# Kernel optimization log

Hardware: AMD Instinct MI355X
Metric: run time of the kernel (lower is better)

The kernel has to match this reference:

```python
import jax, jax.numpy as jnp
import numpy as np

N_NODES = 100000
N_EDGES = 1600000
MOTIF_DIM = 32
HIDDEN = 64


def setup_inputs() -> dict:
    key = jax.random.key(0)
    k1, k2, k3, k4 = jax.random.split(key, 4)
    motif_x = jax.random.normal(k1, (N_NODES, MOTIF_DIM), dtype=jnp.float32)
    edge_index = jax.random.randint(k2, (2, N_EDGES), 0, N_NODES, dtype=jnp.int64)
    in_dim = 4 * MOTIF_DIM
    W1 = jax.random.normal(k3, (in_dim, HIDDEN), dtype=jnp.float32) / np.sqrt(in_dim)
    b1 = jnp.zeros((HIDDEN,), dtype=jnp.float32)
    W2 = jax.random.normal(k4, (HIDDEN, 1), dtype=jnp.float32) / np.sqrt(HIDDEN)
    b2 = jnp.zeros((1,), dtype=jnp.float32)
    return {"motif_x": motif_x, "edge_index": edge_index, "W1": W1, "b1": b1, "W2": W2, "b2": b2}


def reference(motif_x, edge_index, W1, b1, W2, b2):
    src = edge_index[0]
    dst = edge_index[1]
    mu = motif_x[src]                      # [E, D] gather
    mv = motif_x[dst]                      # [E, D] gather
    feats = jnp.concatenate([mu, mv, jnp.abs(mu - mv), mu * mv], axis=1)  # [E, 4D]
    h = jax.nn.relu(feats @ W1 + b1)       # [E, H]
    g = jax.nn.sigmoid(h @ W2 + b2)[:, 0]  # [E]
    return jnp.clip(g, 0.0, 1.0)
```

## Files before the change

### kernel.cpp

```cpp
#include <hip/hip_runtime.h>

#define D 32
#define H 64

typedef __attribute__((ext_vector_type(8))) short bf16x8;
typedef __attribute__((ext_vector_type(4))) float f32x4;

__device__ __forceinline__ short f2bf_s(float f) {
  unsigned u = __float_as_uint(f);
  u += 0x7fffu + ((u >> 16) & 1u);
  return (short)(u >> 16);
}
__device__ __forceinline__ float bf2f(short s) {
  return __uint_as_float(((unsigned)(unsigned short)s) << 16);
}

__global__ __launch_bounds__(256) void pack_x(
    const float* __restrict__ x, short* __restrict__ xbf, int n4) {
  int t = blockIdx.x * 256 + threadIdx.x;
  if (t >= n4) return;
  float4 v = ((const float4*)x)[t];
  short4 o;
  o.x = f2bf_s(v.x); o.y = f2bf_s(v.y); o.z = f2bf_s(v.z); o.w = f2bf_s(v.w);
  ((short4*)xbf)[t] = o;
}

__global__ __launch_bounds__(256) void build_btab(
    const float* __restrict__ W1, short* __restrict__ btab) {
  int id = blockIdx.x * 256 + threadIdx.x;
  if (id >= 16 * 64 * 8) return;
  int j = id & 7;
  int l = (id >> 3) & 63;
  int f = id >> 9;
  int s = f & 3, t = f >> 2;
  int k = s * 32 + (l >> 4) * 8 + j;
  int n = t * 16 + (l & 15);
  btab[id] = f2bf_s(W1[k * H + n]);
}

__global__ __launch_bounds__(256) void edge_mfma(
    const short* __restrict__ xbf, const short* __restrict__ btab,
    const int* __restrict__ ei,
    const float* __restrict__ b1, const float* __restrict__ W2,
    const float* __restrict__ b2, float* __restrict__ out,
    int nE, int nTiles) {
  int lane = threadIdx.x & 63;
  int wid  = (blockIdx.x * 256 + threadIdx.x) >> 6;
  int nW   = (gridDim.x * 256) >> 6;
  int m = lane & 15;
  int q = lane >> 4;

  bf16x8 B[16];
#pragma unroll
  for (int f = 0; f < 16; ++f)
    B[f] = *(const bf16x8*)(btab + (f * 64 + lane) * 8);

  float b1v[4], w2v[4];
#pragma unroll
  for (int t = 0; t < 4; ++t) { b1v[t] = b1[t * 16 + m]; w2v[t] = W2[t * 16 + m]; }
  float bias2 = b2[0];

  for (int tile = wid; tile < nTiles; tile += nW) {
    int e  = tile * 16 + m;
    int ec = e < nE ? e : nE - 1;
    int s  = ei[ec];
    int dd = ei[ec + nE];

    bf16x8 amu = *(const bf16x8*)(xbf + s  * D + q * 8);
    bf16x8 amv = *(const bf16x8*)(xbf + dd * D + q * 8);
    bf16x8 ac, ap;
#pragma unroll
    for (int j = 0; j < 8; ++j) {
      float a = bf2f(amu[j]), b = bf2f(amv[j]);
      ac[j] = f2bf_s(fabsf(a - b));
      ap[j] = f2bf_s(a * b);
    }

    float part[4] = {0.f, 0.f, 0.f, 0.f};
#pragma unroll
    for (int t = 0; t < 4; ++t) {
      f32x4 acc = {0.f, 0.f, 0.f, 0.f};
      acc = __builtin_amdgcn_mfma_f32_16x16x32_bf16(amu, B[t * 4 + 0], acc, 0, 0, 0);
      acc = __builtin_amdgcn_mfma_f32_16x16x32_bf16(amv, B[t * 4 + 1], acc, 0, 0, 0);
      acc = __builtin_amdgcn_mfma_f32_16x16x32_bf16(ac,  B[t * 4 + 2], acc, 0, 0, 0);
      acc = __builtin_amdgcn_mfma_f32_16x16x32_bf16(ap,  B[t * 4 + 3], acc, 0, 0, 0);
#pragma unroll
      for (int r = 0; r < 4; ++r) {
        float h = acc[r] + b1v[t];
        part[r] = fmaf(fmaxf(h, 0.f), w2v[t], part[r]);
      }
    }
#pragma unroll
    for (int mask = 1; mask < 16; mask <<= 1)
#pragma unroll
      for (int r = 0; r < 4; ++r)
        part[r] += __shfl_xor(part[r], mask, 64);

    if (m < 4) {
      int ew = tile * 16 + q * 4 + m;
      if (ew < nE) {
        float z = part[m] + bias2;
        float g = 1.f / (1.f + __expf(-z));
        out[ew] = fminf(fmaxf(g, 0.f), 1.f);
      }
    }
  }
}

__global__ __launch_bounds__(256) void edge_full(
    const float* __restrict__ x, const int* __restrict__ ei,
    const float* __restrict__ W1, const float* __restrict__ b1,
    const float* __restrict__ W2, const float* __restrict__ b2,
    float* __restrict__ out, int nE) {
  int e = blockIdx.x * 256 + threadIdx.x;
  if (e >= nE) return;
  int s = ei[e];
  int d = ei[e + nE];
  const float4* mu4 = (const float4*)(x + (size_t)s * D);
  const float4* mv4 = (const float4*)(x + (size_t)d * D);
  float mu[D], mv[D], c[D], p[D];
#pragma unroll
  for (int qq = 0; qq < D / 4; ++qq) {
    float4 a = mu4[qq];
    float4 b = mv4[qq];
    mu[4*qq+0] = a.x; mv[4*qq+0] = b.x; c[4*qq+0] = fabsf(a.x-b.x); p[4*qq+0] = a.x*b.x;
    mu[4*qq+1] = a.y; mv[4*qq+1] = b.y; c[4*qq+1] = fabsf(a.y-b.y); p[4*qq+1] = a.y*b.y;
    mu[4*qq+2] = a.z; mv[4*qq+2] = b.z; c[4*qq+2] = fabsf(a.z-b.z); p[4*qq+2] = a.z*b.z;
    mu[4*qq+3] = a.w; mv[4*qq+3] = b.w; c[4*qq+3] = fabsf(a.w-b.w); p[4*qq+3] = a.w*b.w;
  }
  float z = b2[0];
  for (int j = 0; j < H; ++j) {
    float a = b1[j];
#pragma unroll
    for (int k = 0; k < D; ++k) {
      a = fmaf(mu[k], W1[k * H + j], a);
      a = fmaf(mv[k], W1[(D + k) * H + j], a);
      a = fmaf(c[k],  W1[(2 * D + k) * H + j], a);
      a = fmaf(p[k],  W1[(3 * D + k) * H + j], a);
    }
    a = fmaxf(a, 0.f);
    z = fmaf(a, W2[j], z);
  }
  float g = 1.f / (1.f + __expf(-z));
  out[e] = fminf(fmaxf(g, 0.f), 1.f);
}

extern "C" void kernel_launch(void* const* d_in, const int* in_sizes, int n_in,
                              void* d_out, int out_size, void* d_ws, size_t ws_size,
                              hipStream_t stream) {
  const float* x  = (const float*)d_in[0];
  const int*   ei = (const int*)d_in[1];
  const float* W1 = (const float*)d_in[2];
  const float* b1 = (const float*)d_in[3];
  const float* W2 = (const float*)d_in[4];
  const float* b2 = (const float*)d_in[5];
  float* out = (float*)d_out;

  int nN = in_sizes[0] / D;
  int nE = in_sizes[1] / 2;

  size_t xbf_shorts = (size_t)nN * D;
  size_t need = (xbf_shorts + 16 * 64 * 8) * sizeof(short);
  if (ws_size >= need) {
    short* xbf  = (short*)d_ws;
    short* btab = xbf + xbf_shorts;
    int n4 = nN * D / 4;
    pack_x<<<(n4 + 255) / 256, 256, 0, stream>>>(x, xbf, n4);
    build_btab<<<(16 * 64 * 8 + 255) / 256, 256, 0, stream>>>(W1, btab);
    int nTiles = (nE + 15) / 16;
    edge_mfma<<<2048, 256, 0, stream>>>(xbf, btab, ei, b1, W2, b2, out, nE, nTiles);
  } else {
    edge_full<<<(nE + 255) / 256, 256, 0, stream>>>(x, ei, W1, b1, W2, b2, out, nE);
  }
}
```

Before: 132.0 us.

## Prefetch next tile's gathers, fuse prep kernels, fold bias into MFMA accumulator

The edge kernel now software-pipelines the loop: each iteration issues the index loads and bf16 row gathers for the next tile before computing the current one, hiding gather latency behind the MFMAs. The two preparation kernels are merged into one launch to save a kernel launch. The b1 bias now seeds the MFMA accumulator, and the abs-difference and product operands are built with packed bit tricks and byte permutes instead of per-element conversions. The prefetch raises register pressure, which may lower occupancy.

```diff
diff --git a/kernel.cpp b/kernel.cpp
--- a/kernel.cpp
+++ b/kernel.cpp
@@ -5,37 +5,43 @@
 
 typedef __attribute__((ext_vector_type(8))) short bf16x8;
 typedef __attribute__((ext_vector_type(4))) float f32x4;
+
+union AB { uint4 u; bf16x8 v; };
 
 __device__ __forceinline__ short f2bf_s(float f) {
   unsigned u = __float_as_uint(f);
   u += 0x7fffu + ((u >> 16) & 1u);
   return (short)(u >> 16);
 }
-__device__ __forceinline__ float bf2f(short s) {
-  return __uint_as_float(((unsigned)(unsigned short)s) << 16);
-}
-
-__global__ __launch_bounds__(256) void pack_x(
-    const float* __restrict__ x, short* __restrict__ xbf, int n4) {
-  int t = blockIdx.x * 256 + threadIdx.x;
-  if (t >= n4) return;
-  float4 v = ((const float4*)x)[t];
-  short4 o;
-  o.x = f2bf_s(v.x); o.y = f2bf_s(v.y); o.z = f2bf_s(v.z); o.w = f2bf_s(v.w);
-  ((short4*)xbf)[t] = o;
-}
-
-__global__ __launch_bounds__(256) void build_btab(
-    const float* __restrict__ W1, short* __restrict__ btab) {
-  int id = blockIdx.x * 256 + threadIdx.x;
-  if (id >= 16 * 64 * 8) return;
-  int j = id & 7;
-  int l = (id >> 3) & 63;
-  int f = id >> 9;
-  int s = f & 3, t = f >> 2;
-  int k = s * 32 + (l >> 4) * 8 + j;
-  int n = t * 16 + (l & 15);
-  btab[id] = f2bf_s(W1[k * H + n]);
+
+__device__ __forceinline__ unsigned pack_bf2(float lo, float hi) {
+  return __builtin_amdgcn_perm(__float_as_uint(hi), __float_as_uint(lo), 0x07060302u);
+}
+
+__global__ __launch_bounds__(256) void prep(
+    const float* __restrict__ x, const float* __restrict__ W1,
+    short* __restrict__ xbf, short* __restrict__ btab, int n4, int nPack) {
+  int b = blockIdx.x;
+  if (b < nPack) {
+    int i = b * 256 + threadIdx.x;
+    if (i < n4) {
+      float4 v = ((const float4*)x)[i];
+      short4 o;
+      o.x = f2bf_s(v.x); o.y = f2bf_s(v.y); o.z = f2bf_s(v.z); o.w = f2bf_s(v.w);
+      ((short4*)xbf)[i] = o;
+    }
+  } else {
+    int id = (b - nPack) * 256 + threadIdx.x;
+    if (id < 16 * 64 * 8) {
+      int j = id & 7;
+      int l = (id >> 3) & 63;
+      int f = id >> 9;
+      int s = f & 3, t = f >> 2;
+      int k = s * 32 + (l >> 4) * 8 + j;
+      int n = t * 16 + (l & 15);
+      btab[id] = f2bf_s(W1[k * H + n]);
+    }
+  }
 }
 
 __global__ __launch_bounds__(256) void edge_mfma(
@@ -50,46 +56,71 @@
   int m = lane & 15;
   int q = lane >> 4;
 
+  if (wid >= nTiles) return;
+
   bf16x8 B[16];
 #pragma unroll
   for (int f = 0; f < 16; ++f)
     B[f] = *(const bf16x8*)(btab + (f * 64 + lane) * 8);
 
-  float b1v[4], w2v[4];
-#pragma unroll
-  for (int t = 0; t < 4; ++t) { b1v[t] = b1[t * 16 + m]; w2v[t] = W2[t * 16 + m]; }
+  f32x4 bias[4];
+  float w2v[4];
+#pragma unroll
+  for (int t = 0; t < 4; ++t) {
+    float bv = b1[t * 16 + m];
+    bias[t] = (f32x4){bv, bv, bv, bv};
+    w2v[t] = W2[t * 16 + m];
+  }
   float bias2 = b2[0];
 
-  for (int tile = wid; tile < nTiles; tile += nW) {
-    int e  = tile * 16 + m;
+  const uint4* xb = (const uint4*)xbf;
+
+  AB mu, mv, mun, mvn;
+  {
+    int e = wid * 16 + m;
     int ec = e < nE ? e : nE - 1;
-    int s  = ei[ec];
-    int dd = ei[ec + nE];
-
-    bf16x8 amu = *(const bf16x8*)(xbf + s  * D + q * 8);
-    bf16x8 amv = *(const bf16x8*)(xbf + dd * D + q * 8);
-    bf16x8 ac, ap;
-#pragma unroll
-    for (int j = 0; j < 8; ++j) {
-      float a = bf2f(amu[j]), b = bf2f(amv[j]);
-      ac[j] = f2bf_s(fabsf(a - b));
-      ap[j] = f2bf_s(a * b);
-    }
-
-    float part[4] = {0.f, 0.f, 0.f, 0.f};
+    int s = ei[ec], dd = ei[ec + nE];
+    mu.u = xb[s * 4 + q];
+    mv.u = xb[dd * 4 + q];
+  }
+
+  for (int tile = wid; tile < nTiles; ) {
+    int nxt = tile + nW;
+    if (nxt < nTiles) {
+      int e = nxt * 16 + m;
+      int ec = e < nE ? e : nE - 1;
+      int s = ei[ec], dd = ei[ec + nE];
+      mun.u = xb[s * 4 + q];
+      mvn.u = xb[dd * 4 + q];
+    }
+
+    AB ac, ap;
+#pragma unroll
+    for (int k = 0; k < 4; ++k) {
+      unsigned a = (&mu.u.x)[k], b = (&mv.u.x)[k];
+      float alo = __uint_as_float(a << 16);
+      float ahi = __uint_as_float(a & 0xffff0000u);
+      float blo = __uint_as_float(b << 16);
+      float bhi = __uint_as_float(b & 0xffff0000u);
+      (&ac.u.x)[k] = pack_bf2(fabsf(alo - blo), fabsf(ahi - bhi));
+      (&ap.u.x)[k] = pack_bf2(alo * blo, ahi * bhi);
+    }
+
+    float part[4];
 #pragma unroll
     for (int t = 0; t < 4; ++t) {
-      f32x4 acc = {0.f, 0.f, 0.f, 0.f};
-      acc = __builtin_amdgcn_mfma_f32_16x16x32_bf16(amu, B[t * 4 + 0], acc, 0, 0, 0);
-      acc = __builtin_amdgcn_mfma_f32_16x16x32_bf16(amv, B[t * 4 + 1], acc, 0, 0, 0);
-      acc = __builtin_amdgcn_mfma_f32_16x16x32_bf16(ac,  B[t * 4 + 2], acc, 0, 0, 0);
-      acc = __builtin_amdgcn_mfma_f32_16x16x32_bf16(ap,  B[t * 4 + 3], acc, 0, 0, 0);
+      f32x4 acc = bias[t];
+      acc = __builtin_amdgcn_mfma_f32_16x16x32_bf16(mu.v, B[t * 4 + 0], acc, 0, 0, 0);
+      acc = __builtin_amdgcn_mfma_f32_16x16x32_bf16(mv.v, B[t * 4 + 1], acc, 0, 0, 0);
+      acc = __builtin_amdgcn_mfma_f32_16x16x32_bf16(ac.v, B[t * 4 + 2], acc, 0, 0, 0);
+      acc = __builtin_amdgcn_mfma_f32_16x16x32_bf16(ap.v, B[t * 4 + 3], acc, 0, 0, 0);
 #pragma unroll
       for (int r = 0; r < 4; ++r) {
-        float h = acc[r] + b1v[t];
-        part[r] = fmaf(fmaxf(h, 0.f), w2v[t], part[r]);
+        float h = fmaxf(acc[r], 0.f);
+        part[r] = (t == 0) ? h * w2v[0] : fmaf(h, w2v[t], part[r]);
       }
     }
+
 #pragma unroll
     for (int mask = 1; mask < 16; mask <<= 1)
 #pragma unroll
@@ -104,6 +135,9 @@
         out[ew] = fminf(fmaxf(g, 0.f), 1.f);
       }
     }
+
+    mu = mun; mv = mvn;
+    tile = nxt;
   }
 }
 
@@ -165,8 +199,9 @@
     short* xbf  = (short*)d_ws;
     short* btab = xbf + xbf_shorts;
     int n4 = nN * D / 4;
-    pack_x<<<(n4 + 255) / 256, 256, 0, stream>>>(x, xbf, n4);
-    build_btab<<<(16 * 64 * 8 + 255) / 256, 256, 0, stream>>>(W1, btab);
+    int nPack = (n4 + 255) / 256;
+    int nBt = (16 * 64 * 8 + 255) / 256;
+    prep<<<nPack + nBt, 256, 0, stream>>>(x, W1, xbf, btab, n4, nPack);
     int nTiles = (nE + 15) / 16;
     edge_mfma<<<2048, 256, 0, stream>>>(xbf, btab, ei, b1, W2, b2, out, nE, nTiles);
   } else {
```

Result: no change. 130.1 us (-1.4%).
